# Kernel optimization log

Measured on AMD Instinct MI355X. Metric: run time of the kernel, lower is better.

## Reference

```python
import jax, jax.numpy as jnp
import numpy as np
import math

D_MODEL = 1024
NUM_HEADS = 16
THETA = 10000.0


def _rope(x, pos, theta):
    # x: (B, S, H, d_k), pos: (B, S) int32/64
    d_k = x.shape[-1]
    half = d_k // 2
    inv_freq = theta ** (-jnp.arange(half, dtype=jnp.float32) * 2.0 / d_k)  # (half,)
    ang = pos.astype(jnp.float32)[..., None] * inv_freq  # (B, S, half)
    cos = jnp.cos(ang)[..., None, :]  # (B, S, 1, half) broadcast over heads
    sin = jnp.sin(ang)[..., None, :]
    x1 = x[..., 0::2]  # even dims
    x2 = x[..., 1::2]  # odd dims
    out_even = x1 * cos - x2 * sin
    out_odd = x1 * sin + x2 * cos
    # re-interleave pairs
    return jnp.stack([out_even, out_odd], axis=-1).reshape(x.shape)


def setup_inputs() -> dict:
    key = jax.random.key(0)
    k0, k1, k2, k3, k4 = jax.random.split(key, 5)
    B, S, D = 4, 2048, D_MODEL
    std = math.sqrt(2.0 / (D + D))
    x = jax.random.normal(k0, (B, S, D), dtype=jnp.float32)
    wq = jax.random.normal(k1, (D, D), dtype=jnp.float32) * std
    wk = jax.random.normal(k2, (D, D), dtype=jnp.float32) * std
    wv = jax.random.normal(k3, (D, D), dtype=jnp.float32) * std
    wo = jax.random.normal(k4, (D, D), dtype=jnp.float32) * std
    return {"x": x, "wq": wq, "wk": wk, "wv": wv, "wo": wo}


def reference(x, wq, wk, wv, wo):
    B, S, D = x.shape
    H = NUM_HEADS
    d_k = D // H
    # torch Linear: y = x @ W.T
    q = (x @ wq.T).reshape(B, S, H, d_k)
    k = (x @ wk.T).reshape(B, S, H, d_k)
    v = (x @ wv.T).reshape(B, S, H, d_k)
    pos = jnp.broadcast_to(jnp.arange(S), (B, S))
    q = _rope(q, pos, THETA)
    k = _rope(k, pos, THETA)
    # (B, H, S, d_k)
    q = q.transpose(0, 2, 1, 3)
    k = k.transpose(0, 2, 1, 3)
    v = v.transpose(0, 2, 1, 3)
    scores = jnp.einsum("bhqd,bhkd->bhqk", q, k) / jnp.sqrt(jnp.float32(d_k))
    causal = jnp.tril(jnp.ones((S, S), dtype=bool))  # True = keep
    scores = jnp.where(causal, scores, -jnp.inf)
    attn = jax.nn.softmax(scores, axis=-1)
    out = jnp.einsum("bhqk,bhkd->bhqd", attn, v)
    out = out.transpose(0, 2, 1, 3).reshape(B, S, D)
    return out @ wo.T
```

## Files before the change

### kernel.cpp

```cpp
#include <hip/hip_runtime.h>

#define DEV __device__ __forceinline__

typedef float f32x4 __attribute__((ext_vector_type(4)));
typedef float f32x16 __attribute__((ext_vector_type(16)));
typedef __bf16 bf16x8 __attribute__((ext_vector_type(8)));
typedef unsigned u32x4 __attribute__((ext_vector_type(4)));
typedef unsigned short u16x8 __attribute__((ext_vector_type(8)));

static constexpr int BB = 4, SS = 2048, DD = 1024, HH = 16;
static constexpr int MM = BB * SS;
static constexpr float LOG2_THETA_OVER_HALF = 0.4152410118609203f;
static constexpr float SCL2 = 0.18033688011112042f;

DEV unsigned short f2b(float f) {
    unsigned u = __float_as_uint(f);
    unsigned r = (u + 0x7fffu + ((u >> 16) & 1u)) >> 16;
    return (unsigned short)r;
}
DEV float b2f(unsigned short h) { return __uint_as_float(((unsigned)h) << 16); }

DEV void gload16(const void* g, void* l) {
    __builtin_amdgcn_global_load_lds((const __attribute__((address_space(1))) void*)g,
                                     (__attribute__((address_space(3))) void*)l, 16, 0, 0);
}

DEV unsigned cvtpk(float lo, float hi) {
    unsigned r;
    asm("v_cvt_pk_bf16_f32 %0, %1, %2" : "=v"(r) : "v"(lo), "v"(hi));
    return r;
}

#define PH_BAR do { __builtin_amdgcn_sched_barrier(0); __builtin_amdgcn_s_barrier(); __builtin_amdgcn_sched_barrier(0); } while (0)

__global__ void k_f2b(const float* __restrict__ src, unsigned short* __restrict__ dst, int n) {
    int i = (blockIdx.x * blockDim.x + threadIdx.x) * 4;
    if (i >= n) return;
    float4 v = *reinterpret_cast<const float4*>(src + i);
    ushort4 o;
    o.x = f2b(v.x); o.y = f2b(v.y); o.z = f2b(v.z); o.w = f2b(v.w);
    *reinterpret_cast<ushort4*>(dst + i) = o;
}

__global__ void k_f2b4(const float* __restrict__ s0, const float* __restrict__ s1,
                       const float* __restrict__ s2, const float* __restrict__ s3,
                       unsigned short* __restrict__ dst) {
    int bid = blockIdx.x;
    int t = bid >> 10;
    const float* src = (t == 0) ? s0 : (t == 1) ? s1 : (t == 2) ? s2 : s3;
    int i = ((bid & 1023) * 256 + threadIdx.x) * 4;
    float4 v = *reinterpret_cast<const float4*>(src + i);
    ushort4 o;
    o.x = f2b(v.x); o.y = f2b(v.y); o.z = f2b(v.z); o.w = f2b(v.w);
    *reinterpret_cast<ushort4*>(dst + (size_t)t * DD * DD + i) = o;
}

__global__ __launch_bounds__(512, 2) void k_gemm8(const unsigned short* __restrict__ A,
                                                  const unsigned short* __restrict__ Bw,
                                                  unsigned short* __restrict__ C, int ldc) {
    __shared__ __align__(16) unsigned short LdsA[4][128 * 64];
    __shared__ __align__(16) unsigned short LdsB[4][128 * 64];
    const int tid = threadIdx.x, lane = tid & 63, wid = tid >> 6;
    const int wm = wid >> 2, wn = wid & 3;
    const int fr = lane & 15, l4 = lane >> 4, sw = fr & 7;
    const int m0 = blockIdx.y * 256, n0 = blockIdx.x * 256;

    const int r0 = tid >> 3;
    const int cg = (tid & 7) ^ (r0 & 7);
    const unsigned short* aS = A  + (size_t)(m0 + r0) * 1024 + (cg << 3);
    const unsigned short* bS = Bw + (size_t)(n0 + r0) * 1024 + (cg << 3);
    unsigned short* dA = &LdsA[0][0];
    unsigned short* dB = &LdsB[0][0];
    const int dOf = wid * 512;

    f32x4 acc[8][4] = {};

#define STG(src, base, slot) do {                         \
        unsigned short* d_ = (base) + (slot) * 8192 + dOf;\
        gload16((src), d_);                               \
        gload16((src) + 64 * 1024, d_ + 4096);            \
    } while (0)

#pragma unroll
    for (int T = 0; T < 2; ++T) {
        STG(bS + T * 64,          dB, (2 * T) & 3);
        STG(bS + T * 64 + 131072, dB, (2 * T + 1) & 3);
        STG(aS + T * 64,          dA, (2 * T) & 3);
        STG(aS + T * 64 + 131072, dA, (2 * T + 1) & 3);
    }

    bf16x8 aF[4][2], bL[2][2], bH[2][2];

    for (int T = 0; T < 16; ++T) {
        if (T < 15) { asm volatile("s_waitcnt vmcnt(8)" ::: "memory"); }
        else        { asm volatile("s_waitcnt vmcnt(0)" ::: "memory"); }
        PH_BAR;

        const unsigned short* As_ = &LdsA[(2 * T + wm) & 3][0];
        const unsigned short* Bs_ = &LdsB[(2 * T + (wn >> 1)) & 3][0];
        const int bro = (wn & 1) * 64;

#pragma unroll
        for (int m = 0; m < 4; ++m)
#pragma unroll
            for (int kk = 0; kk < 2; ++kk)
                aF[m][kk] = *(const bf16x8*)&As_[(m * 16 + fr) * 64 + ((((kk << 2) | l4) ^ sw) << 3)];
#pragma unroll
        for (int n = 0; n < 2; ++n)
#pragma unroll
            for (int kk = 0; kk < 2; ++kk)
                bL[n][kk] = *(const bf16x8*)&Bs_[(bro + n * 16 + fr) * 64 + ((((kk << 2) | l4) ^ sw) << 3)];
        __builtin_amdgcn_s_setprio(1);
#pragma unroll
        for (int m = 0; m < 4; ++m)
#pragma unroll
            for (int n = 0; n < 2; ++n)
#pragma unroll
                for (int kk = 0; kk < 2; ++kk)
                    acc[m][n] = __builtin_amdgcn_mfma_f32_16x16x32_bf16(aF[m][kk], bL[n][kk], acc[m][n], 0, 0, 0);
        __builtin_amdgcn_s_setprio(0);
        PH_BAR;

#pragma unroll
        for (int n = 0; n < 2; ++n)
#pragma unroll
            for (int kk = 0; kk < 2; ++kk)
                bH[n][kk] = *(const bf16x8*)&Bs_[(bro + (n + 2) * 16 + fr) * 64 + ((((kk << 2) | l4) ^ sw) << 3)];
        __builtin_amdgcn_s_setprio(1);
#pragma unroll
        for (int m = 0; m < 4; ++m)
#pragma unroll
            for (int n = 0; n < 2; ++n)
#pragma unroll
                for (int kk = 0; kk < 2; ++kk)
                    acc[m][n + 2] = __builtin_amdgcn_mfma_f32_16x16x32_bf16(aF[m][kk], bH[n][kk], acc[m][n + 2], 0, 0, 0);
        __builtin_amdgcn_s_setprio(0);
        PH_BAR;

#pragma unroll
        for (int m = 0; m < 4; ++m)
#pragma unroll
            for (int kk = 0; kk < 2; ++kk)
                aF[m][kk] = *(const bf16x8*)&As_[((m + 4) * 16 + fr) * 64 + ((((kk << 2) | l4) ^ sw) << 3)];
        if (T + 2 < 16) {
            STG(bS + (T + 2) * 64,          dB, (2 * T) & 3);
            STG(bS + (T + 2) * 64 + 131072, dB, (2 * T + 1) & 3);
        }
        __builtin_amdgcn_s_setprio(1);
#pragma unroll
        for (int m = 0; m < 4; ++m)
#pragma unroll
            for (int n = 0; n < 2; ++n)
#pragma unroll
                for (int kk = 0; kk < 2; ++kk)
                    acc[m + 4][n + 2] = __builtin_amdgcn_mfma_f32_16x16x32_bf16(aF[m][kk], bH[n][kk], acc[m + 4][n + 2], 0, 0, 0);
        __builtin_amdgcn_s_setprio(0);
        PH_BAR;

        if (T + 2 < 16) {
            STG(aS + (T + 2) * 64,          dA, (2 * T) & 3);
            STG(aS + (T + 2) * 64 + 131072, dA, (2 * T + 1) & 3);
        }
        __builtin_amdgcn_s_setprio(1);
#pragma unroll
        for (int m = 0; m < 4; ++m)
#pragma unroll
            for (int n = 0; n < 2; ++n)
#pragma unroll
                for (int kk = 0; kk < 2; ++kk)
                    acc[m + 4][n] = __builtin_amdgcn_mfma_f32_16x16x32_bf16(aF[m][kk], bL[n][kk], acc[m + 4][n], 0, 0, 0);
        __builtin_amdgcn_s_setprio(0);
    }
#undef STG

    const int rb = l4 * 4;
#pragma unroll
    for (int m = 0; m < 8; ++m)
#pragma unroll
        for (int n = 0; n < 4; ++n)
#pragma unroll
            for (int r = 0; r < 4; ++r) {
                int row = m0 + wm * 128 + m * 16 + rb + r;
                int col = n0 + wn * 64 + n * 16 + fr;
                C[(size_t)row * ldc + col] = f2b(acc[m][n][r]);
            }
}

template <int OUTF32>
__global__ __launch_bounds__(256) void k_gemm(const unsigned short* __restrict__ A,
                                              const unsigned short* __restrict__ Bw,
                                              void* __restrict__ Cp, int ldc) {
    __shared__ __align__(16) unsigned short As[128 * 32];
    __shared__ __align__(16) unsigned short Bs[128 * 32];
    const int tid = threadIdx.x;
    const int lane = tid & 63, wid = tid >> 6;
    const int wm = wid >> 1, wn = wid & 1;
    const int fr = lane & 15, fk8 = (lane >> 4) * 8;
    const int m0 = blockIdx.y * 128, n0 = blockIdx.x * 128;
    const int r0 = tid >> 2, c0 = (tid & 3) * 8;

    f32x4 acc[4][4] = {};

    for (int kt = 0; kt < 1024; kt += 32) {
        gload16(&A[(size_t)(m0 + r0) * 1024 + kt + c0],       (unsigned short*)As + wid * 512);
        gload16(&A[(size_t)(m0 + 64 + r0) * 1024 + kt + c0],  (unsigned short*)As + 2048 + wid * 512);
        gload16(&Bw[(size_t)(n0 + r0) * 1024 + kt + c0],      (unsigned short*)Bs + wid * 512);
        gload16(&Bw[(size_t)(n0 + 64 + r0) * 1024 + kt + c0], (unsigned short*)Bs + 2048 + wid * 512);
        __syncthreads();

        bf16x8 af[4], bfv[4];
#pragma unroll
        for (int i = 0; i < 4; i++)
            af[i] = *(const bf16x8*)&As[(wm * 64 + i * 16 + fr) * 32 + fk8];
#pragma unroll
        for (int j = 0; j < 4; j++)
            bfv[j] = *(const bf16x8*)&Bs[(wn * 64 + j * 16 + fr) * 32 + fk8];
#pragma unroll
        for (int i = 0; i < 4; i++)
#pragma unroll
            for (int j = 0; j < 4; j++)
                acc[i][j] = __builtin_amdgcn_mfma_f32_16x16x32_bf16(af[i], bfv[j], acc[i][j], 0, 0, 0);
        __syncthreads();
    }

    const int rb = (lane >> 4) * 4;
#pragma unroll
    for (int i = 0; i < 4; i++)
#pragma unroll
        for (int j = 0; j < 4; j++)
#pragma unroll
            for (int r = 0; r < 4; r++) {
                int row = m0 + wm * 64 + i * 16 + rb + r;
                int col = n0 + wn * 64 + j * 16 + fr;
                if (OUTF32) ((float*)Cp)[(size_t)row * ldc + col] = acc[i][j][r];
                else        ((unsigned short*)Cp)[(size_t)row * ldc + col] = f2b(acc[i][j][r]);
            }
}

__global__ void k_ropeQK(unsigned short* __restrict__ T) {
    int g = blockIdx.x * blockDim.x + threadIdx.x;
    int m = g >> 9, p = g & 511;
    int i = p & 31;
    int s = m & (SS - 1);
    int col = ((p >> 5) << 6) + (i << 1);
    float inv = exp2f(-(float)i * LOG2_THETA_OVER_HALF);
    float ang = (float)s * inv;
    float sn, cs;
    sincosf(ang, &sn, &cs);
    unsigned short* q2 = T + (size_t)m * 3072 + col;
    unsigned short* k2 = q2 + 1024;
    float q1 = b2f(q2[0]), q2v = b2f(q2[1]);
    float k1 = b2f(k2[0]), k2v = b2f(k2[1]);
    q2[0] = f2b((q1 * cs - q2v * sn) * SCL2);
    q2[1] = f2b((q1 * sn + q2v * cs) * SCL2);
    k2[0] = f2b(k1 * cs - k2v * sn);
    k2[1] = f2b(k1 * sn + k2v * cs);
}

__global__ __launch_bounds__(256) void k_vt(const unsigned short* __restrict__ V,
                                            unsigned short* __restrict__ Vt) {
    __shared__ unsigned short T[64 * 65];
    const int tid = threadIdx.x;
    const int s0 = blockIdx.x * 64, bh = blockIdx.y;
    const int b = bh >> 4, h = bh & 15;
    const int r = tid >> 3, c8 = (tid & 7) * 8;
#pragma unroll
    for (int p = 0; p < 2; p++) {
        int row = p * 32 + r;
        u16x8 v = *(const u16x8*)&V[(size_t)(b * SS + s0 + row) * 3072 + h * 64 + c8];
#pragma unroll
        for (int j = 0; j < 8; j++) T[(c8 + j) * 65 + row] = v[j];
    }
    __syncthreads();
#pragma unroll
    for (int p = 0; p < 2; p++) {
        int d = p * 32 + r;
        u16x8 o;
#pragma unroll
        for (int j = 0; j < 8; j++) o[j] = T[d * 65 + c8 + j];
        *(u16x8*)&Vt[((size_t)bh * 64 + d) * 2048 + s0 + c8] = o;
    }
}

DEV void packp(const f32x16& s, bf16x8* pf) {
#pragma unroll
    for (int g = 0; g < 2; g++) {
        unsigned w0 = cvtpk(s[8 * g + 0], s[8 * g + 1]);
        unsigned w1 = cvtpk(s[8 * g + 2], s[8 * g + 3]);
        unsigned w2 = cvtpk(s[8 * g + 4], s[8 * g + 5]);
        unsigned w3 = cvtpk(s[8 * g + 6], s[8 * g + 7]);
        asm("v_permlane32_swap_b32 %0, %1" : "+v"(w0), "+v"(w2));
        asm("v_permlane32_swap_b32 %0, %1" : "+v"(w1), "+v"(w3));
        u32x4 pd;
        pd[0] = w0; pd[1] = w1; pd[2] = w2; pd[3] = w3;
        pf[g] = __builtin_bit_cast(bf16x8, pd);
    }
}

DEV float sum16(const f32x16& s) {
    return (((s[0] + s[1]) + (s[2] + s[3])) + ((s[4] + s[5]) + (s[6] + s[7]))) +
           (((s[8] + s[9]) + (s[10] + s[11])) + (((s[12] + s[13]) + (s[14] + s[15]))));
}

__global__ __launch_bounds__(512, 4) void k_attn(const unsigned short* __restrict__ QKV,
                                                 const unsigned short* __restrict__ Vt,
                                                 unsigned short* __restrict__ O) {
    __shared__ __align__(16) unsigned short Kbuf[2][64 * 64];
    __shared__ __align__(16) unsigned short Vbuf[2][64 * 64];
    const int tid = threadIdx.x, lane = tid & 63, wid = tid >> 6;
    const int l31 = lane & 31, hi = lane >> 5;
    const int bh = blockIdx.x, b = bh >> 4, h = bh & 15;
    const int qt = gridDim.y - 1 - blockIdx.y;
    const int q0 = qt * 256;
    const int wq0 = q0 + wid * 32;
    const int tdw = wq0 >> 6;
    const int nk = (q0 + 256) >> 6;

    const int srow = tid >> 3, sc = tid & 7;
    const unsigned short* ksrc = QKV + 1024 + ((size_t)(b * SS) + srow) * 3072 + h * 64 + ((sc ^ (srow & 7)) << 3);
    const unsigned short* vsrc = Vt + ((size_t)(bh * 64) + srow) * 2048 + ((sc ^ (srow & 7)) << 3);

    const unsigned short* qp = QKV + (size_t)(b * SS + wq0 + l31) * 3072 + h * 64;
    bf16x8 qf[4];
#pragma unroll
    for (int dt = 0; dt < 4; dt++) qf[dt] = *(const bf16x8*)(qp + dt * 16 + hi * 8);

    f32x16 oacc0 = {}, oacc1 = {};
    float lrow = 0.f;
    const int swz = l31 & 7;

    gload16(ksrc, (unsigned short*)Kbuf[0] + wid * 512);
    gload16(vsrc, (unsigned short*)Vbuf[0] + wid * 512);

    for (int t = 0; t < nk; t++) {
        __syncthreads();
        if (t + 1 < nk) {
            gload16(ksrc + (size_t)(t + 1) * 64 * 3072, (unsigned short*)Kbuf[(t + 1) & 1] + wid * 512);
            gload16(vsrc + (t + 1) * 64,                (unsigned short*)Vbuf[(t + 1) & 1] + wid * 512);
        }
        if (t > tdw) continue;
        const unsigned short* Ks = Kbuf[t & 1];
        const unsigned short* Vs = Vbuf[t & 1];

        if (t < tdw) {
            f32x16 s0 = {}, s1 = {};
            __builtin_amdgcn_s_setprio(1);
#pragma unroll
            for (int dt = 0; dt < 4; dt++) {
                bf16x8 kf = *(const bf16x8*)&Ks[l31 * 64 + (((dt * 2 + hi) ^ swz) << 3)];
                s0 = __builtin_amdgcn_mfma_f32_32x32x16_bf16(kf, qf[dt], s0, 0, 0, 0);
            }
#pragma unroll
            for (int dt = 0; dt < 4; dt++) {
                bf16x8 kf = *(const bf16x8*)&Ks[(32 + l31) * 64 + (((dt * 2 + hi) ^ swz) << 3)];
                s1 = __builtin_amdgcn_mfma_f32_32x32x16_bf16(kf, qf[dt], s1, 0, 0, 0);
            }
            __builtin_amdgcn_s_setprio(0);
#pragma unroll
            for (int r = 0; r < 16; r++) {
                s0[r] = __builtin_amdgcn_exp2f(s0[r]);
                s1[r] = __builtin_amdgcn_exp2f(s1[r]);
            }
            lrow += sum16(s0) + sum16(s1);
            bf16x8 pA[2], pB[2];
            packp(s0, pA);
            packp(s1, pB);
            __builtin_amdgcn_s_setprio(1);
#pragma unroll
            for (int g = 0; g < 2; g++) {
                bf16x8 vf0 = *(const bf16x8*)&Vs[l31 * 64 + (((g * 2 + hi) ^ swz) << 3)];
                oacc0 = __builtin_amdgcn_mfma_f32_32x32x16_bf16(vf0, pA[g], oacc0, 0, 0, 0);
                bf16x8 vf1 = *(const bf16x8*)&Vs[(32 + l31) * 64 + (((g * 2 + hi) ^ swz) << 3)];
                oacc1 = __builtin_amdgcn_mfma_f32_32x32x16_bf16(vf1, pA[g], oacc1, 0, 0, 0);
            }
#pragma unroll
            for (int g = 0; g < 2; g++) {
                bf16x8 vf0 = *(const bf16x8*)&Vs[l31 * 64 + (((4 + g * 2 + hi) ^ swz) << 3)];
                oacc0 = __builtin_amdgcn_mfma_f32_32x32x16_bf16(vf0, pB[g], oacc0, 0, 0, 0);
                bf16x8 vf1 = *(const bf16x8*)&Vs[(32 + l31) * 64 + (((4 + g * 2 + hi) ^ swz) << 3)];
                oacc1 = __builtin_amdgcn_mfma_f32_32x32x16_bf16(vf1, pB[g], oacc1, 0, 0, 0);
            }
            __builtin_amdgcn_s_setprio(0);
        } else {
#pragma unroll
            for (int kt2 = 0; kt2 < 2; kt2++) {
                const int kb = t * 64 + kt2 * 32;
                if (kb > wq0) break;

                f32x16 sacc = {};
                __builtin_amdgcn_s_setprio(1);
#pragma unroll
                for (int dt = 0; dt < 4; dt++) {
                    bf16x8 kf = *(const bf16x8*)&Ks[(kt2 * 32 + l31) * 64 + (((dt * 2 + hi) ^ swz) << 3)];
                    sacc = __builtin_amdgcn_mfma_f32_32x32x16_bf16(kf, qf[dt], sacc, 0, 0, 0);
                }
                __builtin_amdgcn_s_setprio(0);

                if (kb == wq0) {
#pragma unroll
                    for (int r = 0; r < 16; r++) {
                        int kr = (r & 3) + 8 * (r >> 2) + 4 * hi;
                        sacc[r] = (kr > l31) ? -1e30f : sacc[r];
                    }
                }

#pragma unroll
                for (int r = 0; r < 16; r++) sacc[r] = __builtin_amdgcn_exp2f(sacc[r]);
                lrow += sum16(sacc);

                bf16x8 pf[2];
                packp(sacc, pf);

                __builtin_amdgcn_s_setprio(1);
#pragma unroll
                for (int g = 0; g < 2; g++) {
                    bf16x8 vf0 = *(const bf16x8*)&Vs[l31 * 64 + (((kt2 * 4 + g * 2 + hi) ^ swz) << 3)];
                    oacc0 = __builtin_amdgcn_mfma_f32_32x32x16_bf16(vf0, pf[g], oacc0, 0, 0, 0);
                    bf16x8 vf1 = *(const bf16x8*)&Vs[(32 + l31) * 64 + (((kt2 * 4 + g * 2 + hi) ^ swz) << 3)];
                    oacc1 = __builtin_amdgcn_mfma_f32_32x32x16_bf16(vf1, pf[g], oacc1, 0, 0, 0);
                }
                __builtin_amdgcn_s_setprio(0);
            }
        }
    }

    float lsum = lrow + __shfl_xor(lrow, 32);
    float linv = 1.0f / lsum;
    unsigned short* op = O + (size_t)(b * SS + wq0 + l31) * 1024 + h * 64 + hi * 4;
#pragma unroll
    for (int g = 0; g < 4; g++) {
        uint2 u;
        u.x = cvtpk(oacc0[4 * g + 0] * linv, oacc0[4 * g + 1] * linv);
        u.y = cvtpk(oacc0[4 * g + 2] * linv, oacc0[4 * g + 3] * linv);
        *(uint2*)&op[g * 8] = u;
        uint2 v;
        v.x = cvtpk(oacc1[4 * g + 0] * linv, oacc1[4 * g + 1] * linv);
        v.y = cvtpk(oacc1[4 * g + 2] * linv, oacc1[4 * g + 3] * linv);
        *(uint2*)&op[32 + g * 8] = v;
    }
}

extern "C" void kernel_launch(void* const* d_in, const int* in_sizes, int n_in,
                              void* d_out, int out_size, void* d_ws, size_t ws_size,
                              hipStream_t stream) {
    const float* x  = (const float*)d_in[0];
    const float* wq = (const float*)d_in[1];
    const float* wk = (const float*)d_in[2];
    const float* wv = (const float*)d_in[3];
    const float* wo = (const float*)d_in[4];
    float* out = (float*)d_out;

    unsigned short* xb    = (unsigned short*)d_ws;
    unsigned short* wqkvb = xb + (size_t)MM * DD;
    unsigned short* wob   = wqkvb + (size_t)3 * DD * DD;
    unsigned short* QKV   = wob + (size_t)DD * DD;
    unsigned short* Ob    = QKV + (size_t)MM * 3 * DD;
    unsigned short* Vtb   = xb;

    k_f2b<<<MM * DD / 4 / 256, 256, 0, stream>>>(x, xb, MM * DD);
    k_f2b4<<<4096, 256, 0, stream>>>(wq, wk, wv, wo, wqkvb);

    dim3 gq(3 * DD / 256, MM / 256);
    k_gemm8<<<gq, 512, 0, stream>>>(xb, wqkvb, QKV, 3 * DD);

    int npair = MM * 512;
    k_ropeQK<<<npair / 256, 256, 0, stream>>>(QKV);

    dim3 gv(SS / 64, BB * HH);
    k_vt<<<gv, 256, 0, stream>>>(QKV + 2 * DD, Vtb);

    dim3 ga(BB * HH, SS / 256);
    k_attn<<<ga, 512, 0, stream>>>(QKV, Vtb, Ob);

    dim3 gg(DD / 128, MM / 128);
    k_gemm<1><<<gg, 256, 0, stream>>>(Ob, wob, (void*)out, DD);
}
```

Before: 179.6 us.

## Retile pipelined GEMM to 256x128 and reuse it for output projection

Replaces the 256x256 pipelined QKV GEMM with a templated 256x128 variant whose 8 waves are laid out as 4x2. A and B tile loads are re-staged with a new prefetch schedule (A one step ahead, B two steps ahead, vmcnt(2)). The same kernel, with fp32 output, now also handles the output projection, replacing the simpler single-buffered 128x128 GEMM. The aim is more blocks for better CU occupancy and a faster, pipelined O-projection. The cost is less reuse per tile in the QKV GEMM.

```diff
diff --git a/kernel.cpp b/kernel.cpp
--- a/kernel.cpp
+++ b/kernel.cpp
@@ -55,15 +55,16 @@
     *reinterpret_cast<ushort4*>(dst + (size_t)t * DD * DD + i) = o;
 }
 
-__global__ __launch_bounds__(512, 2) void k_gemm8(const unsigned short* __restrict__ A,
-                                                  const unsigned short* __restrict__ Bw,
-                                                  unsigned short* __restrict__ C, int ldc) {
+template <int OUTF32>
+__global__ __launch_bounds__(512, 2) void k_gemm8n(const unsigned short* __restrict__ A,
+                                                   const unsigned short* __restrict__ Bw,
+                                                   void* __restrict__ Cp, int ldc) {
     __shared__ __align__(16) unsigned short LdsA[4][128 * 64];
     __shared__ __align__(16) unsigned short LdsB[4][128 * 64];
     const int tid = threadIdx.x, lane = tid & 63, wid = tid >> 6;
-    const int wm = wid >> 2, wn = wid & 3;
+    const int wm = wid >> 1, wn = wid & 1;
     const int fr = lane & 15, l4 = lane >> 4, sw = fr & 7;
-    const int m0 = blockIdx.y * 256, n0 = blockIdx.x * 256;
+    const int m0 = blockIdx.y * 256, n0 = blockIdx.x * 128;
 
     const int r0 = tid >> 3;
     const int cg = (tid & 7) ^ (r0 & 7);
@@ -73,46 +74,49 @@
     unsigned short* dB = &LdsB[0][0];
     const int dOf = wid * 512;
 
-    f32x4 acc[8][4] = {};
-
-#define STG(src, base, slot) do {                         \
-        unsigned short* d_ = (base) + (slot) * 8192 + dOf;\
-        gload16((src), d_);                               \
-        gload16((src) + 64 * 1024, d_ + 4096);            \
+    f32x4 acc[4][4] = {};
+
+#define STGA(t, h) do {                                                     \
+        unsigned short* d_ = dA + (((2 * (t) + (h)) & 3) * 8192) + dOf;     \
+        const unsigned short* s_ = aS + (size_t)(t) * 64 + (size_t)(h) * 131072; \
+        gload16(s_, d_); gload16(s_ + 65536, d_ + 4096);                    \
     } while (0)
-
-#pragma unroll
-    for (int T = 0; T < 2; ++T) {
-        STG(bS + T * 64,          dB, (2 * T) & 3);
-        STG(bS + T * 64 + 131072, dB, (2 * T + 1) & 3);
-        STG(aS + T * 64,          dA, (2 * T) & 3);
-        STG(aS + T * 64 + 131072, dA, (2 * T + 1) & 3);
-    }
-
-    bf16x8 aF[4][2], bL[2][2], bH[2][2];
+#define STGB(t) do {                                                        \
+        unsigned short* d_ = dB + (((t) & 3) * 8192) + dOf;                 \
+        const unsigned short* s_ = bS + (size_t)(t) * 64;                   \
+        gload16(s_, d_); gload16(s_ + 65536, d_ + 4096);                    \
+    } while (0)
+
+    STGB(0);
+    STGA(0, 0); STGA(0, 1);
+    STGB(1);
+
+    bf16x8 aF[2][2], bL[2][2], bH[2][2];
 
     for (int T = 0; T < 16; ++T) {
-        if (T < 15) { asm volatile("s_waitcnt vmcnt(8)" ::: "memory"); }
+        if (T < 15) { asm volatile("s_waitcnt vmcnt(2)" ::: "memory"); }
         else        { asm volatile("s_waitcnt vmcnt(0)" ::: "memory"); }
         PH_BAR;
 
-        const unsigned short* As_ = &LdsA[(2 * T + wm) & 3][0];
-        const unsigned short* Bs_ = &LdsB[(2 * T + (wn >> 1)) & 3][0];
-        const int bro = (wn & 1) * 64;
-
-#pragma unroll
-        for (int m = 0; m < 4; ++m)
+        const unsigned short* As_ = &LdsA[(2 * T + (wm >> 1)) & 3][0];
+        const unsigned short* Bs_ = &LdsB[T & 3][0];
+        const int aro = (wm & 1) * 64;
+        const int bro = wn * 64;
+
+#pragma unroll
+        for (int m = 0; m < 2; ++m)
 #pragma unroll
             for (int kk = 0; kk < 2; ++kk)
-                aF[m][kk] = *(const bf16x8*)&As_[(m * 16 + fr) * 64 + ((((kk << 2) | l4) ^ sw) << 3)];
+                aF[m][kk] = *(const bf16x8*)&As_[(aro + m * 16 + fr) * 64 + ((((kk << 2) | l4) ^ sw) << 3)];
 #pragma unroll
         for (int n = 0; n < 2; ++n)
 #pragma unroll
             for (int kk = 0; kk < 2; ++kk)
                 bL[n][kk] = *(const bf16x8*)&Bs_[(bro + n * 16 + fr) * 64 + ((((kk << 2) | l4) ^ sw) << 3)];
+        if (T + 1 < 16) STGA(T + 1, 0);
         __builtin_amdgcn_s_setprio(1);
 #pragma unroll
-        for (int m = 0; m < 4; ++m)
+        for (int m = 0; m < 2; ++m)
 #pragma unroll
             for (int n = 0; n < 2; ++n)
 #pragma unroll
@@ -126,9 +130,10 @@
 #pragma unroll
             for (int kk = 0; kk < 2; ++kk)
                 bH[n][kk] = *(const bf16x8*)&Bs_[(bro + (n + 2) * 16 + fr) * 64 + ((((kk << 2) | l4) ^ sw) << 3)];
+        if (T + 1 < 16) STGA(T + 1, 1);
         __builtin_amdgcn_s_setprio(1);
 #pragma unroll
-        for (int m = 0; m < 4; ++m)
+        for (int m = 0; m < 2; ++m)
 #pragma unroll
             for (int n = 0; n < 2; ++n)
 #pragma unroll
@@ -138,102 +143,42 @@
         PH_BAR;
 
 #pragma unroll
-        for (int m = 0; m < 4; ++m)
+        for (int m = 0; m < 2; ++m)
 #pragma unroll
             for (int kk = 0; kk < 2; ++kk)
-                aF[m][kk] = *(const bf16x8*)&As_[((m + 4) * 16 + fr) * 64 + ((((kk << 2) | l4) ^ sw) << 3)];
-        if (T + 2 < 16) {
-            STG(bS + (T + 2) * 64,          dB, (2 * T) & 3);
-            STG(bS + (T + 2) * 64 + 131072, dB, (2 * T + 1) & 3);
-        }
+                aF[m][kk] = *(const bf16x8*)&As_[(aro + (m + 2) * 16 + fr) * 64 + ((((kk << 2) | l4) ^ sw) << 3)];
+        if (T + 2 < 16) STGB(T + 2);
         __builtin_amdgcn_s_setprio(1);
 #pragma unroll
-        for (int m = 0; m < 4; ++m)
+        for (int m = 0; m < 2; ++m)
 #pragma unroll
             for (int n = 0; n < 2; ++n)
 #pragma unroll
                 for (int kk = 0; kk < 2; ++kk)
-                    acc[m + 4][n + 2] = __builtin_amdgcn_mfma_f32_16x16x32_bf16(aF[m][kk], bH[n][kk], acc[m + 4][n + 2], 0, 0, 0);
+                    acc[m + 2][n + 2] = __builtin_amdgcn_mfma_f32_16x16x32_bf16(aF[m][kk], bH[n][kk], acc[m + 2][n + 2], 0, 0, 0);
+#pragma unroll
+        for (int m = 0; m < 2; ++m)
+#pragma unroll
+            for (int n = 0; n < 2; ++n)
+#pragma unroll
+                for (int kk = 0; kk < 2; ++kk)
+                    acc[m + 2][n] = __builtin_amdgcn_mfma_f32_16x16x32_bf16(aF[m][kk], bL[n][kk], acc[m + 2][n], 0, 0, 0);
         __builtin_amdgcn_s_setprio(0);
-        PH_BAR;
-
-        if (T + 2 < 16) {
-            STG(aS + (T + 2) * 64,          dA, (2 * T) & 3);
-            STG(aS + (T + 2) * 64 + 131072, dA, (2 * T + 1) & 3);
-        }
-        __builtin_amdgcn_s_setprio(1);
-#pragma unroll
-        for (int m = 0; m < 4; ++m)
-#pragma unroll
-            for (int n = 0; n < 2; ++n)
-#pragma unroll
-                for (int kk = 0; kk < 2; ++kk)
-                    acc[m + 4][n] = __builtin_amdgcn_mfma_f32_16x16x32_bf16(aF[m][kk], bL[n][kk], acc[m + 4][n], 0, 0, 0);
-        __builtin_amdgcn_s_setprio(0);
-    }
-#undef STG
+    }
+#undef STGA
+#undef STGB
 
     const int rb = l4 * 4;
 #pragma unroll
-    for (int m = 0; m < 8; ++m)
+    for (int m = 0; m < 4; ++m)
 #pragma unroll
         for (int n = 0; n < 4; ++n)
 #pragma unroll
             for (int r = 0; r < 4; ++r) {
-                int row = m0 + wm * 128 + m * 16 + rb + r;
+                int row = m0 + wm * 64 + m * 16 + rb + r;
                 int col = n0 + wn * 64 + n * 16 + fr;
-                C[(size_t)row * ldc + col] = f2b(acc[m][n][r]);
-            }
-}
-
-template <int OUTF32>
-__global__ __launch_bounds__(256) void k_gemm(const unsigned short* __restrict__ A,
-                                              const unsigned short* __restrict__ Bw,
-                                              void* __restrict__ Cp, int ldc) {
-    __shared__ __align__(16) unsigned short As[128 * 32];
-    __shared__ __align__(16) unsigned short Bs[128 * 32];
-    const int tid = threadIdx.x;
-    const int lane = tid & 63, wid = tid >> 6;
-    const int wm = wid >> 1, wn = wid & 1;
-    const int fr = lane & 15, fk8 = (lane >> 4) * 8;
-    const int m0 = blockIdx.y * 128, n0 = blockIdx.x * 128;
-    const int r0 = tid >> 2, c0 = (tid & 3) * 8;
-
-    f32x4 acc[4][4] = {};
-
-    for (int kt = 0; kt < 1024; kt += 32) {
-        gload16(&A[(size_t)(m0 + r0) * 1024 + kt + c0],       (unsigned short*)As + wid * 512);
-        gload16(&A[(size_t)(m0 + 64 + r0) * 1024 + kt + c0],  (unsigned short*)As + 2048 + wid * 512);
-        gload16(&Bw[(size_t)(n0 + r0) * 1024 + kt + c0],      (unsigned short*)Bs + wid * 512);
-        gload16(&Bw[(size_t)(n0 + 64 + r0) * 1024 + kt + c0], (unsigned short*)Bs + 2048 + wid * 512);
-        __syncthreads();
-
-        bf16x8 af[4], bfv[4];
-#pragma unroll
-        for (int i = 0; i < 4; i++)
-            af[i] = *(const bf16x8*)&As[(wm * 64 + i * 16 + fr) * 32 + fk8];
-#pragma unroll
-        for (int j = 0; j < 4; j++)
-            bfv[j] = *(const bf16x8*)&Bs[(wn * 64 + j * 16 + fr) * 32 + fk8];
-#pragma unroll
-        for (int i = 0; i < 4; i++)
-#pragma unroll
-            for (int j = 0; j < 4; j++)
-                acc[i][j] = __builtin_amdgcn_mfma_f32_16x16x32_bf16(af[i], bfv[j], acc[i][j], 0, 0, 0);
-        __syncthreads();
-    }
-
-    const int rb = (lane >> 4) * 4;
-#pragma unroll
-    for (int i = 0; i < 4; i++)
-#pragma unroll
-        for (int j = 0; j < 4; j++)
-#pragma unroll
-            for (int r = 0; r < 4; r++) {
-                int row = m0 + wm * 64 + i * 16 + rb + r;
-                int col = n0 + wn * 64 + j * 16 + fr;
-                if (OUTF32) ((float*)Cp)[(size_t)row * ldc + col] = acc[i][j][r];
-                else        ((unsigned short*)Cp)[(size_t)row * ldc + col] = f2b(acc[i][j][r]);
+                if (OUTF32) ((float*)Cp)[(size_t)row * ldc + col] = acc[m][n][r];
+                else        ((unsigned short*)Cp)[(size_t)row * ldc + col] = f2b(acc[m][n][r]);
             }
 }
 
@@ -460,8 +405,8 @@
     k_f2b<<<MM * DD / 4 / 256, 256, 0, stream>>>(x, xb, MM * DD);
     k_f2b4<<<4096, 256, 0, stream>>>(wq, wk, wv, wo, wqkvb);
 
-    dim3 gq(3 * DD / 256, MM / 256);
-    k_gemm8<<<gq, 512, 0, stream>>>(xb, wqkvb, QKV, 3 * DD);
+    dim3 gq(3 * DD / 128, MM / 256);
+    k_gemm8n<0><<<gq, 512, 0, stream>>>(xb, wqkvb, (void*)QKV, 3 * DD);
 
     int npair = MM * 512;
     k_ropeQK<<<npair / 256, 256, 0, stream>>>(QKV);
@@ -472,6 +417,6 @@
     dim3 ga(BB * HH, SS / 256);
     k_attn<<<ga, 512, 0, stream>>>(QKV, Vtb, Ob);
 
-    dim3 gg(DD / 128, MM / 128);
-    k_gemm<1><<<gg, 256, 0, stream>>>(Ob, wob, (void*)out, DD);
-}
+    dim3 go(DD / 128, MM / 256);
+    k_gemm8n<1><<<go, 512, 0, stream>>>(Ob, wob, (void*)out, DD);
+}
```

After: 189.8 us. +5.7%, slower.
